# Performance work log

Hardware: AMD Instinct MI355X
Metric: run time of the kernel (lower is better)

Reference implementation:

```python
import jax, jax.numpy as jnp
import numpy as np

HIDDEN = 1024
OUT = 512
N = 8192


def setup_inputs() -> dict:
    key = jax.random.key(0)
    ks = jax.random.split(key, 12)
    s_h = 1.0 / np.sqrt(HIDDEN)
    s_o = 1.0 / np.sqrt(OUT)
    return {
        "za": jax.random.normal(ks[0], (N, HIDDEN), jnp.float32),
        "zb": jax.random.normal(ks[1], (N, HIDDEN), jnp.float32),
        # proj: Linear(HIDDEN,HIDDEN) -> ELU -> Linear(HIDDEN,OUT)
        "W1": jax.random.normal(ks[2], (HIDDEN, HIDDEN), jnp.float32) * s_h,
        "b1": jax.random.normal(ks[3], (HIDDEN,), jnp.float32) * s_h,
        "W2": jax.random.normal(ks[4], (HIDDEN, OUT), jnp.float32) * s_h,
        "b2": jax.random.normal(ks[5], (OUT,), jnp.float32) * s_h,
        # CrossAttention Linears on OUT dim (shared for both directions)
        "Wq": jax.random.normal(ks[6], (OUT, OUT), jnp.float32) * s_o,
        "bq": jax.random.normal(ks[7], (OUT,), jnp.float32) * s_o,
        "Wk": jax.random.normal(ks[8], (OUT, OUT), jnp.float32) * s_o,
        "bk": jax.random.normal(ks[9], (OUT,), jnp.float32) * s_o,
        "Wv": jax.random.normal(ks[10], (OUT, OUT), jnp.float32) * s_o,
        "bv": jax.random.normal(ks[11], (OUT,), jnp.float32) * s_o,
    }


def _cross_attn(q_in, k_in, v_in, Wq, bq, Wk, bk, Wv, bv, scale):
    Q = q_in @ Wq + bq  # [N, D]
    K = k_in @ Wk + bk
    V = v_in @ Wv + bv
    scores = (Q @ K.T) / scale  # [N, N]
    attn = jax.nn.softmax(scores, axis=-1)
    return attn @ V  # [N, D]


def reference(za, zb, W1, b1, W2, b2, Wq, bq, Wk, bk, Wv, bv):
    scale = jnp.sqrt(jnp.asarray(OUT / 2, jnp.float32))  # sqrt(hidden_dim/2) of attn dim

    def proj(x):
        return jax.nn.elu(x @ W1 + b1) @ W2 + b2

    za_p = proj(za)  # [N, OUT]
    zb_p = proj(zb)
    za_ca = _cross_attn(za_p, zb_p, zb_p, Wq, bq, Wk, bk, Wv, bv, scale)
    zb_ca = _cross_attn(zb_p, za_p, za_p, Wq, bq, Wk, bk, Wv, bv, scale)
    return jnp.concatenate((za_ca, zb_ca), axis=1)  # [N, 2*OUT]
```

## Files before the change

### kernel.cpp

```cpp
#include <hip/hip_runtime.h>
#include <hip/hip_bf16.h>
#include <stdint.h>

#define HIDDEN 1024
#define OUTD   512
#define NSEQ   8192
#define MTOT   16384

typedef unsigned short u16;
typedef __attribute__((ext_vector_type(8))) short short8;
typedef __attribute__((ext_vector_type(4))) float f32x4;

__device__ __forceinline__ u16 f2b(float f){
  union { __hip_bfloat16 h; u16 u; } c; c.h = __float2bfloat16(f); return c.u;
}

__device__ __forceinline__ void gload_lds16(const void* g, void* l){
  __builtin_amdgcn_global_load_lds(
    (const __attribute__((address_space(1))) uint32_t*)(uintptr_t)g,
    (__attribute__((address_space(3))) uint32_t*)(uintptr_t)l, 16, 0, 0);
}

#define MFMA16(a,b,c) __builtin_amdgcn_mfma_f32_16x16x32_bf16((a),(b),(c),0,0,0)

__global__ void cvt_bf16_kernel(const float* __restrict__ in, u16* __restrict__ out, int n4){
  int i = blockIdx.x*blockDim.x + threadIdx.x;
  int stride = gridDim.x*blockDim.x;
  for (; i < n4; i += stride){
    float4 v = ((const float4*)in)[i];
    ushort4 o;
    o.x = f2b(v.x); o.y = f2b(v.y); o.z = f2b(v.z); o.w = f2b(v.w);
    ((ushort4*)out)[i] = o;
  }
}

__global__ void transpose_bf16_kernel(const float* __restrict__ in, u16* __restrict__ out, int R, int C){
  __shared__ float t[32][33];
  int tx = threadIdx.x, ty = threadIdx.y;
  int c0 = blockIdx.x*32, r0 = blockIdx.y*32;
  #pragma unroll
  for (int i = ty; i < 32; i += 8) t[i][tx] = in[(size_t)(r0+i)*C + c0 + tx];
  __syncthreads();
  #pragma unroll
  for (int i = ty; i < 32; i += 8) out[(size_t)(c0+i)*R + r0 + tx] = f2b(t[tx][i]);
}

template<bool ELU_ACT, bool BIAS_ROW>
__global__ __launch_bounds__(256, 2) void gemm_bt(
    const u16* __restrict__ A, const u16* __restrict__ BT,
    const float* __restrict__ bias, u16* __restrict__ C,
    int M, int N, int K, float outscale)
{
  __shared__ u16 As[128*32];
  __shared__ u16 Bs[128*32];
  const int tid = threadIdx.x;
  const int w = tid >> 6, l = tid & 63;
  const int lr = l & 15, lg = l >> 4;
  const int brow = blockIdx.y * 128, bcol = blockIdx.x * 128;
  const int wr = w >> 1, wc = w & 1;
  f32x4 acc[4][4];
  #pragma unroll
  for (int i=0;i<4;i++)
    #pragma unroll
    for (int j=0;j<4;j++) acc[i][j] = f32x4{0.f,0.f,0.f,0.f};

  for (int k0 = 0; k0 < K; k0 += 32){
    __syncthreads();
    {
      int sb = w*64;
      int s0 = sb + l;
      int s1 = 256 + sb + l;
      gload_lds16(A  + (size_t)(brow + (s0>>2))*K + k0 + (s0&3)*8, As + sb*8);
      gload_lds16(A  + (size_t)(brow + (s1>>2))*K + k0 + (s1&3)*8, As + (256+sb)*8);
      gload_lds16(BT + (size_t)(bcol + (s0>>2))*K + k0 + (s0&3)*8, Bs + sb*8);
      gload_lds16(BT + (size_t)(bcol + (s1>>2))*K + k0 + (s1&3)*8, Bs + (256+sb)*8);
    }
    __syncthreads();
    short8 a[4], b[4];
    #pragma unroll
    for (int i=0;i<4;i++){
      a[i] = *(const short8*)(As + (wr*64 + i*16 + lr)*32 + lg*8);
      b[i] = *(const short8*)(Bs + (wc*64 + i*16 + lr)*32 + lg*8);
    }
    #pragma unroll
    for (int i=0;i<4;i++)
      #pragma unroll
      for (int j=0;j<4;j++)
        acc[i][j] = MFMA16(a[i], b[j], acc[i][j]);
  }

  #pragma unroll
  for (int i=0;i<4;i++)
    #pragma unroll
    for (int j=0;j<4;j++){
      int col = bcol + wc*64 + j*16 + lr;
      float bc = BIAS_ROW ? 0.f : bias[col];
      #pragma unroll
      for (int r=0;r<4;r++){
        int row = brow + wr*64 + i*16 + lg*4 + r;
        float v = acc[i][j][r] + (BIAS_ROW ? bias[row] : bc);
        if (ELU_ACT) v = v > 0.f ? v : expm1f(v);
        v *= outscale;
        C[(size_t)row*N + col] = f2b(v);
      }
    }
}

__global__ __launch_bounds__(512, 2) void flash_attn(
    const u16* __restrict__ Qb, const u16* __restrict__ Kb,
    const u16* __restrict__ Vt, float* __restrict__ Opart,
    float2* __restrict__ MLpart)
{
  __shared__ u16 Ks[2][32*512];
  __shared__ u16 Vts[2][512*32];
  __shared__ u16 Plds[8][16*32];
  const int tid = threadIdx.x;
  const int w = tid >> 6, l = tid & 63;
  const int lr = l & 15, lg = l >> 4;
  const int xcd = blockIdx.x & 7;
  const int idx = blockIdx.x >> 3;
  const int dir = xcd >> 2;
  const int half = (xcd >> 1) & 1;
  const int qb  = (xcd & 1)*32 + idx;
  const int qrow0 = dir*NSEQ + qb*128 + w*16;
  const int kv0 = (1-dir)*NSEQ + half*(NSEQ/2);
  const int NT = (NSEQ/2)/32;

  short8 qf[16];
  #pragma unroll
  for (int kt=0; kt<16; kt++)
    qf[kt] = *(const short8*)(Qb + (size_t)(qrow0 + lr)*OUTD + kt*32 + lg*8);

  f32x4 o[32];
  #pragma unroll
  for (int i=0;i<32;i++) o[i] = f32x4{0.f,0.f,0.f,0.f};
  float m = -1e30f, ls = 0.f;

  u16* Pw = &Plds[w][0];

  auto STAGE = [&](int buf, int t){
    u16* Kd = &Ks[buf][0];
    u16* Vd = &Vts[buf][0];
    #pragma unroll
    for (int i=0;i<4;i++){
      int g = w*4 + i;
      gload_lds16(Kb + (size_t)(kv0 + t*32 + g)*OUTD + ((l ^ (g&7))*8), Kd + g*512);
    }
    #pragma unroll
    for (int i=0;i<4;i++){
      int g = w*4 + i;
      int d = g*16 + (l>>2);
      int p = l & 3;
      int fd = (d ^ (d>>2)) & 3;
      gload_lds16(Vt + (size_t)d*MTOT + kv0 + t*32 + ((p ^ fd)*8), Vd + (g*64 + l)*8);
    }
  };

  STAGE(0, 0);
  __syncthreads();

  for (int t=0; t<NT; t++){
    const int cur = t & 1;
    if (t+1 < NT) STAGE(cur^1, t+1);

    const u16* Kc = &Ks[cur][0];
    const u16* Vc = &Vts[cur][0];

    f32x4 s0 = f32x4{0.f,0.f,0.f,0.f}, s1 = s0;
    __builtin_amdgcn_s_setprio(1);
    #pragma unroll
    for (int kt=0; kt<16; kt++){
      short8 ka = *(const short8*)(Kc + (size_t)(lr)*512    + (((kt*4+lg) ^ (lr&7))*8));
      short8 kb = *(const short8*)(Kc + (size_t)(16+lr)*512 + (((kt*4+lg) ^ (lr&7))*8));
      s0 = MFMA16(ka, qf[kt], s0);
      s1 = MFMA16(kb, qf[kt], s1);
    }
    __builtin_amdgcn_s_setprio(0);

    float mx = fmaxf(fmaxf(fmaxf(s0[0],s0[1]), fmaxf(s0[2],s0[3])),
                     fmaxf(fmaxf(s1[0],s1[1]), fmaxf(s1[2],s1[3])));
    mx = fmaxf(mx, __shfl_xor(mx, 16));
    mx = fmaxf(mx, __shfl_xor(mx, 32));
    bool need = mx > m + 8.f;
    if (__any(need)){
      float mn = fmaxf(m, mx);
      float corr = exp2f((m - mn)*1.44269504f);
      m = mn; ls *= corr;
      #pragma unroll
      for (int i=0;i<32;i++){
        o[i][0] *= corr; o[i][1] *= corr; o[i][2] *= corr; o[i][3] *= corr;
      }
    }
    float p0[4], p1[4], sm = 0.f;
    #pragma unroll
    for (int r=0;r<4;r++){
      p0[r] = exp2f((s0[r]-m)*1.44269504f);
      p1[r] = exp2f((s1[r]-m)*1.44269504f);
      sm += p0[r] + p1[r];
    }
    sm += __shfl_xor(sm, 16);
    sm += __shfl_xor(sm, 32);
    ls += sm;

    ushort4 w0, w1;
    w0.x = f2b(p0[0]); w0.y = f2b(p0[1]); w0.z = f2b(p0[2]); w0.w = f2b(p0[3]);
    w1.x = f2b(p1[0]); w1.y = f2b(p1[1]); w1.z = f2b(p1[2]); w1.w = f2b(p1[3]);
    *(ushort4*)(Pw + lr*32 + (((lg>>1) ^ (lr&3))*8)     + (lg&1)*4) = w0;
    *(ushort4*)(Pw + lr*32 + (((2+(lg>>1)) ^ (lr&3))*8) + (lg&1)*4) = w1;

    short8 pb = *(const short8*)(Pw + lr*32 + ((lg ^ (lr&3))*8));
    __builtin_amdgcn_s_setprio(1);
    #pragma unroll
    for (int nj=0; nj<32; nj++){
      int d = nj*16 + lr;
      int fd = (d ^ (d>>2)) & 3;
      short8 va = *(const short8*)(Vc + d*32 + ((lg ^ fd)*8));
      o[nj] = MFMA16(va, pb, o[nj]);
    }
    __builtin_amdgcn_s_setprio(0);

    __syncthreads();
  }

  const int qg = dir*NSEQ + qb*128 + w*16 + lr;
  float* Od = Opart + ((size_t)half*MTOT + qg)*OUTD;
  #pragma unroll
  for (int nj=0; nj<32; nj++)
    *(f32x4*)(Od + nj*16 + lg*4) = o[nj];
  if (lg == 0)
    MLpart[half*MTOT + qg] = make_float2(m, ls);
}

__global__ void merge_kernel(const float* __restrict__ Opart,
                             const float2* __restrict__ MLpart,
                             float* __restrict__ out){
  int i = blockIdx.x*blockDim.x + threadIdx.x;
  int qg = i >> 7, d4 = i & 127;
  float2 ml0 = MLpart[qg], ml1 = MLpart[MTOT + qg];
  float M = fmaxf(ml0.x, ml1.x);
  float w0 = exp2f((ml0.x - M)*1.44269504f);
  float w1 = exp2f((ml1.x - M)*1.44269504f);
  float inv = 1.f / (ml0.y*w0 + ml1.y*w1);
  f32x4 a = ((const f32x4*)Opart)[(size_t)qg*128 + d4];
  f32x4 b = ((const f32x4*)Opart)[(size_t)MTOT*128 + (size_t)qg*128 + d4];
  f32x4 r;
  #pragma unroll
  for (int j=0;j<4;j++) r[j] = (a[j]*w0 + b[j]*w1)*inv;
  int row = qg & (NSEQ-1), dir = qg >> 13;
  ((f32x4*)out)[(size_t)row*256 + dir*128 + d4] = r;
}

#define OFF_W1T  ((size_t)0)
#define OFF_W2T  (OFF_W1T + (size_t)1024*1024*2)
#define OFF_WQT  (OFF_W2T + (size_t)512*1024*2)
#define OFF_WKT  (OFF_WQT + (size_t)512*512*2)
#define OFF_WVT  (OFF_WKT + (size_t)512*512*2)
#define OFF_XC   (OFF_WVT + (size_t)512*512*2)
#define OFF_H    (OFF_XC  + (size_t)MTOT*HIDDEN*2)
#define OFF_P    (OFF_H   + (size_t)MTOT*HIDDEN*2)
#define OFF_QB   OFF_XC
#define OFF_KB   (OFF_XC + (size_t)MTOT*OUTD*2)
#define OFF_VT   OFF_H
#define OFF_ML   (OFF_P  + (size_t)MTOT*OUTD*2)
#define OFF_OP   (OFF_ML + (size_t)2*MTOT*8)

extern "C" void kernel_launch(void* const* d_in, const int* in_sizes, int n_in,
                              void* d_out, int out_size, void* d_ws, size_t ws_size,
                              hipStream_t stream) {
  const float* za = (const float*)d_in[0];
  const float* zb = (const float*)d_in[1];
  const float* W1 = (const float*)d_in[2];
  const float* b1 = (const float*)d_in[3];
  const float* W2 = (const float*)d_in[4];
  const float* b2 = (const float*)d_in[5];
  const float* Wq = (const float*)d_in[6];
  const float* bq = (const float*)d_in[7];
  const float* Wk = (const float*)d_in[8];
  const float* bk = (const float*)d_in[9];
  const float* Wv = (const float*)d_in[10];
  const float* bv = (const float*)d_in[11];
  float* out = (float*)d_out;
  char* ws = (char*)d_ws;

  u16* W1T = (u16*)(ws + OFF_W1T);
  u16* W2T = (u16*)(ws + OFF_W2T);
  u16* WqT = (u16*)(ws + OFF_WQT);
  u16* WkT = (u16*)(ws + OFF_WKT);
  u16* WvT = (u16*)(ws + OFF_WVT);
  u16* Xc  = (u16*)(ws + OFF_XC);
  u16* H   = (u16*)(ws + OFF_H);
  u16* P   = (u16*)(ws + OFF_P);
  u16* Qb  = (u16*)(ws + OFF_QB);
  u16* Kb  = (u16*)(ws + OFF_KB);
  u16* Vt  = (u16*)(ws + OFF_VT);
  float2* ML = (float2*)(ws + OFF_ML);
  float*  OP = (float*)(ws + OFF_OP);

  cvt_bf16_kernel<<<2048, 256, 0, stream>>>(za, Xc, NSEQ*HIDDEN/4);
  cvt_bf16_kernel<<<2048, 256, 0, stream>>>(zb, Xc + (size_t)NSEQ*HIDDEN, NSEQ*HIDDEN/4);
  transpose_bf16_kernel<<<dim3(32,32), dim3(32,8), 0, stream>>>(W1, W1T, 1024, 1024);
  transpose_bf16_kernel<<<dim3(16,32), dim3(32,8), 0, stream>>>(W2, W2T, 1024, 512);
  transpose_bf16_kernel<<<dim3(16,16), dim3(32,8), 0, stream>>>(Wq, WqT, 512, 512);
  transpose_bf16_kernel<<<dim3(16,16), dim3(32,8), 0, stream>>>(Wk, WkT, 512, 512);
  transpose_bf16_kernel<<<dim3(16,16), dim3(32,8), 0, stream>>>(Wv, WvT, 512, 512);

  gemm_bt<true,false><<<dim3(HIDDEN/128, MTOT/128), 256, 0, stream>>>(
      Xc, W1T, b1, H, MTOT, HIDDEN, HIDDEN, 1.f);
  gemm_bt<false,false><<<dim3(OUTD/128, MTOT/128), 256, 0, stream>>>(
      H, W2T, b2, P, MTOT, OUTD, HIDDEN, 1.f);
  gemm_bt<false,false><<<dim3(OUTD/128, MTOT/128), 256, 0, stream>>>(
      P, WqT, bq, Qb, MTOT, OUTD, OUTD, 0.0625f);
  gemm_bt<false,false><<<dim3(OUTD/128, MTOT/128), 256, 0, stream>>>(
      P, WkT, bk, Kb, MTOT, OUTD, OUTD, 1.f);
  gemm_bt<false,true><<<dim3(MTOT/128, OUTD/128), 256, 0, stream>>>(
      WvT, P, bv, Vt, OUTD, MTOT, OUTD, 1.f);

  flash_attn<<<256, 512, 0, stream>>>(Qb, Kb, Vt, OP, ML);
  merge_kernel<<<(MTOT*128)/256, 256, 0, stream>>>(OP, ML, out);
}
```

Measured before the change: 704.2 us.

## Split PV accumulation across waves by head-dim slice with shared P tile

```diff
diff --git a/kernel.cpp b/kernel.cpp
--- a/kernel.cpp
+++ b/kernel.cpp
@@ -113,7 +113,9 @@
 {
   __shared__ u16 Ks[2][32*512];
   __shared__ u16 Vts[2][512*32];
-  __shared__ u16 Plds[8][16*32];
+  __shared__ u16 Plds[128*32];
+  __shared__ float corr_s[128];
+  __shared__ float flag_s[8];
   const int tid = threadIdx.x;
   const int w = tid >> 6, l = tid & 63;
   const int lr = l & 15, lg = l >> 4;
@@ -131,37 +133,41 @@
   for (int kt=0; kt<16; kt++)
     qf[kt] = *(const short8*)(Qb + (size_t)(qrow0 + lr)*OUTD + kt*32 + lg*8);
 
-  f32x4 o[32];
-  #pragma unroll
-  for (int i=0;i<32;i++) o[i] = f32x4{0.f,0.f,0.f,0.f};
+  f32x4 o[4][8];
+  #pragma unroll
+  for (int dt=0;dt<4;dt++)
+    #pragma unroll
+    for (int qt=0;qt<8;qt++) o[dt][qt] = f32x4{0.f,0.f,0.f,0.f};
   float m = -1e30f, ls = 0.f;
 
-  u16* Pw = &Plds[w][0];
-
-  auto STAGE = [&](int buf, int t){
+  const u16* kp[4];
+  const u16* vp[4];
+  #pragma unroll
+  for (int i=0;i<4;i++){
+    int g = w*4 + i;
+    kp[i] = Kb + (size_t)(kv0 + g)*OUTD + ((l ^ (g&7))*8);
+    int d = g*16 + (l>>2);
+    int fd = (d ^ (d>>2)) & 3;
+    vp[i] = Vt + (size_t)d*MTOT + kv0 + (((l&3) ^ fd)*8);
+  }
+
+  auto STAGE = [&](int buf){
     u16* Kd = &Ks[buf][0];
     u16* Vd = &Vts[buf][0];
     #pragma unroll
-    for (int i=0;i<4;i++){
-      int g = w*4 + i;
-      gload_lds16(Kb + (size_t)(kv0 + t*32 + g)*OUTD + ((l ^ (g&7))*8), Kd + g*512);
-    }
-    #pragma unroll
-    for (int i=0;i<4;i++){
-      int g = w*4 + i;
-      int d = g*16 + (l>>2);
-      int p = l & 3;
-      int fd = (d ^ (d>>2)) & 3;
-      gload_lds16(Vt + (size_t)d*MTOT + kv0 + t*32 + ((p ^ fd)*8), Vd + (g*64 + l)*8);
-    }
+    for (int i=0;i<4;i++) gload_lds16(kp[i], Kd + (w*4+i)*512);
+    #pragma unroll
+    for (int i=0;i<4;i++) gload_lds16(vp[i], Vd + ((w*4+i)*64 + l)*8);
+    #pragma unroll
+    for (int i=0;i<4;i++){ kp[i] += 32*OUTD; vp[i] += 32; }
   };
 
-  STAGE(0, 0);
+  STAGE(0);
   __syncthreads();
 
   for (int t=0; t<NT; t++){
     const int cur = t & 1;
-    if (t+1 < NT) STAGE(cur^1, t+1);
+    if (t+1 < NT) STAGE(cur^1);
 
     const u16* Kc = &Ks[cur][0];
     const u16* Vc = &Vts[cur][0];
@@ -181,16 +187,16 @@
                      fmaxf(fmaxf(s1[0],s1[1]), fmaxf(s1[2],s1[3])));
     mx = fmaxf(mx, __shfl_xor(mx, 16));
     mx = fmaxf(mx, __shfl_xor(mx, 32));
-    bool need = mx > m + 8.f;
-    if (__any(need)){
+    float corr = 1.f;
+    bool needany = __any(mx > m + 8.f);
+    if (needany){
       float mn = fmaxf(m, mx);
-      float corr = exp2f((m - mn)*1.44269504f);
+      corr = exp2f((m - mn)*1.44269504f);
       m = mn; ls *= corr;
-      #pragma unroll
-      for (int i=0;i<32;i++){
-        o[i][0] *= corr; o[i][1] *= corr; o[i][2] *= corr; o[i][3] *= corr;
-      }
-    }
+    }
+    if (lg == 0) corr_s[w*16 + lr] = corr;
+    if (l == 0)  flag_s[w] = needany ? 1.f : 0.f;
+
     float p0[4], p1[4], sm = 0.f;
     #pragma unroll
     for (int r=0;r<4;r++){
@@ -202,33 +208,65 @@
     sm += __shfl_xor(sm, 32);
     ls += sm;
 
-    ushort4 w0, w1;
-    w0.x = f2b(p0[0]); w0.y = f2b(p0[1]); w0.z = f2b(p0[2]); w0.w = f2b(p0[3]);
-    w1.x = f2b(p1[0]); w1.y = f2b(p1[1]); w1.z = f2b(p1[2]); w1.w = f2b(p1[3]);
-    *(ushort4*)(Pw + lr*32 + (((lg>>1) ^ (lr&3))*8)     + (lg&1)*4) = w0;
-    *(ushort4*)(Pw + lr*32 + (((2+(lg>>1)) ^ (lr&3))*8) + (lg&1)*4) = w1;
-
-    short8 pb = *(const short8*)(Pw + lr*32 + ((lg ^ (lr&3))*8));
+    {
+      int q = w*16 + lr;
+      ushort4 w0, w1;
+      w0.x = f2b(p0[0]); w0.y = f2b(p0[1]); w0.z = f2b(p0[2]); w0.w = f2b(p0[3]);
+      w1.x = f2b(p1[0]); w1.y = f2b(p1[1]); w1.z = f2b(p1[2]); w1.w = f2b(p1[3]);
+      int T0 = ((lg>>1)     ^ (q&3));
+      int T1 = ((2+(lg>>1)) ^ (q&3));
+      *(ushort4*)(Plds + q*32 + T0*8 + (lg&1)*4) = w0;
+      *(ushort4*)(Plds + q*32 + T1*8 + (lg&1)*4) = w1;
+    }
+    __syncthreads();
+
+    float fsum = flag_s[0]+flag_s[1]+flag_s[2]+flag_s[3]
+               + flag_s[4]+flag_s[5]+flag_s[6]+flag_s[7];
+    if (fsum > 0.f){
+      float cc[8];
+      #pragma unroll
+      for (int qt=0;qt<8;qt++) cc[qt] = corr_s[qt*16 + lr];
+      #pragma unroll
+      for (int dt=0;dt<4;dt++)
+        #pragma unroll
+        for (int qt=0;qt<8;qt++){
+          o[dt][qt][0] *= cc[qt]; o[dt][qt][1] *= cc[qt];
+          o[dt][qt][2] *= cc[qt]; o[dt][qt][3] *= cc[qt];
+        }
+    }
+
     __builtin_amdgcn_s_setprio(1);
-    #pragma unroll
-    for (int nj=0; nj<32; nj++){
-      int d = nj*16 + lr;
+    short8 va[4];
+    #pragma unroll
+    for (int dt=0;dt<4;dt++){
+      int d = w*64 + dt*16 + lr;
       int fd = (d ^ (d>>2)) & 3;
-      short8 va = *(const short8*)(Vc + d*32 + ((lg ^ fd)*8));
-      o[nj] = MFMA16(va, pb, o[nj]);
+      va[dt] = *(const short8*)(Vc + d*32 + ((lg ^ fd)*8));
+    }
+    #pragma unroll
+    for (int qt=0; qt<8; qt++){
+      short8 pb = *(const short8*)(Plds + (qt*16+lr)*32 + ((lg ^ (lr&3))*8));
+      #pragma unroll
+      for (int dt=0;dt<4;dt++)
+        o[dt][qt] = MFMA16(va[dt], pb, o[dt][qt]);
     }
     __builtin_amdgcn_s_setprio(0);
 
     __syncthreads();
   }
 
-  const int qg = dir*NSEQ + qb*128 + w*16 + lr;
-  float* Od = Opart + ((size_t)half*MTOT + qg)*OUTD;
-  #pragma unroll
-  for (int nj=0; nj<32; nj++)
-    *(f32x4*)(Od + nj*16 + lg*4) = o[nj];
-  if (lg == 0)
+  #pragma unroll
+  for (int qt=0; qt<8; qt++){
+    size_t qg = (size_t)(dir*NSEQ + qb*128 + qt*16 + lr);
+    float* row = Opart + ((size_t)half*MTOT + qg)*OUTD + w*64;
+    #pragma unroll
+    for (int dt=0; dt<4; dt++)
+      *(f32x4*)(row + dt*16 + lg*4) = o[dt][qt];
+  }
+  if (lg == 0){
+    int qg = dir*NSEQ + qb*128 + w*16 + lr;
     MLpart[half*MTOT + qg] = make_float2(m, ls);
+  }
 }
 
 __global__ void merge_kernel(const float* __restrict__ Opart,
```

Measured after the change: 738.4 us. +4.9%, slower.
